# Kernel optimization log

Hardware: AMD Instinct MI355X
Metric: run time of the kernel (lower is better)

Reference implementation:

```python
import jax, jax.numpy as jnp
import numpy as np

B, L, T = 512, 512, 128
START, STOP = T - 2, T - 1   # tag_dict: '<START>'->126, '<STOP>'->127
NEG = -10000.0


def setup_inputs() -> dict:
    key = jax.random.key(0)
    k1, k2, k3, k4 = jax.random.split(key, 4)
    feats = jax.random.normal(k1, (B, L, T), dtype=jnp.float32)
    # learned transition matrix, initialized as in CRF.__init__
    trans = jax.random.normal(k2, (T, T), dtype=jnp.float32)
    trans = trans.at[START, :].set(NEG).at[:, STOP].set(NEG)
    tags = jax.random.randint(k3, (B, L), 0, T - 2)          # gold tags, no START/STOP
    lens = jax.random.randint(k4, (B,), 1, L + 1)            # actual lengths in [1, L]
    return {"feats": feats, "transitions": trans, "tags": tags, "lens": lens}


def _crf_loss(feats, transitions, tags, lens):
    Bn, Ln, Tn = feats.shape

    # ---- forward algorithm (log partition) ----
    init = jnp.full((Tn,), NEG, dtype=feats.dtype).at[START].set(0.0)
    fv0 = jnp.broadcast_to(init, (Bn, Tn))

    def step(fv, xs):
        emit, i = xs                                  # emit: [B, T]
        # tag_var[b, next, prev] = emit[b,next] + trans[next,prev] + fv[b,prev]
        tv = emit[:, :, None] + transitions[None, :, :] + fv[:, None, :]
        new = jax.scipy.special.logsumexp(tv, axis=2)  # [B, T]
        # freeze fv once past each sentence's length (== gathering at index lens)
        fv = jnp.where((i < lens)[:, None], new, fv)
        return fv, None

    fv, _ = jax.lax.scan(step, fv0, (jnp.swapaxes(feats, 0, 1), jnp.arange(Ln)))
    terminal = fv + transitions[START][None, :]       # matches original (uses START row)
    forward_score = jax.scipy.special.logsumexp(terminal, axis=1)  # [B]

    # ---- gold sentence score ----
    start_col = jnp.full((Bn, 1), START, dtype=tags.dtype)
    stop_col = jnp.full((Bn, 1), STOP, dtype=tags.dtype)
    pad_start = jnp.concatenate([start_col, tags], axis=1)   # [B, L+1]
    pad_stop = jnp.concatenate([tags, stop_col], axis=1)     # [B, L+1]
    pos = jnp.arange(Ln + 1)[None, :]
    pad_stop = jnp.where(pos >= lens[:, None], STOP, pad_stop)

    trans_terms = transitions[pad_stop, pad_start]           # [B, L+1]
    trans_sum = jnp.sum(jnp.where(pos <= lens[:, None], trans_terms, 0.0), axis=1)
    emit_terms = jnp.take_along_axis(feats, tags[:, :, None], axis=2)[..., 0]  # [B, L]
    emit_mask = jnp.arange(Ln)[None, :] < lens[:, None]
    emit_sum = jnp.sum(jnp.where(emit_mask, emit_terms, 0.0), axis=1)
    gold_score = trans_sum + emit_sum

    return jnp.mean(forward_score - gold_score)


def reference(feats, transitions, tags, lens):
    return _crf_loss(feats, transitions, tags, lens)
```

## Files before the change

### kernel.cpp

```cpp
#include <hip/hip_runtime.h>

#define Bsz 512
#define Lsz 512
#define Tsz 128
#define TAG_START 126
#define TAG_STOP 127

__device__ __forceinline__ float rl(float v, int j) {
  return __int_as_float(__builtin_amdgcn_readlane(__float_as_int(v), j));
}
__device__ __forceinline__ float wave_max(float v) {
  #pragma unroll
  for (int off = 32; off > 0; off >>= 1) v = fmaxf(v, __shfl_down(v, off, 64));
  return v;
}
__device__ __forceinline__ float wave_sum(float v) {
  #pragma unroll
  for (int off = 32; off > 0; off >>= 1) v += __shfl_down(v, off, 64);
  return v;
}

__device__ __forceinline__ void lds_barrier() {
  asm volatile("s_waitcnt lgkmcnt(0)\n\ts_barrier" ::: "memory");
}

__global__ __launch_bounds__(256, 1) void crf_fwd_kernel(
    const float* __restrict__ feats, const float* __restrict__ trans,
    const int* __restrict__ tags, const int* __restrict__ lens,
    float* __restrict__ diff_out)
{
  __shared__ float p_part[2][4][Tsz];
  __shared__ float wredA[4];
  __shared__ float wredB[4];

  const int b   = blockIdx.x;
  const int tid = threadIdx.x;
  const int w   = tid >> 6;
  const int k   = tid & 63;
  const int tagu = w * 32 + (k & 31);
  const int len = lens[b];
  const float* fb = feats + (size_t)b * Lsz * Tsz;

  float er0[32], er1[32];
  {
    const float* r0 = trans + (size_t)k * Tsz + w * 32;
    const float* r1 = trans + (size_t)(k + 64) * Tsz + w * 32;
    #pragma unroll
    for (int j = 0; j < 32; j += 4) {
      float4 a = *(const float4*)(r0 + j);
      float4 c = *(const float4*)(r1 + j);
      er0[j+0] = __expf(a.x); er0[j+1] = __expf(a.y);
      er0[j+2] = __expf(a.z); er0[j+3] = __expf(a.w);
      er1[j+0] = __expf(c.x); er1[j+1] = __expf(c.y);
      er1[j+2] = __expf(c.z); er1[j+3] = __expf(c.w);
    }
  }

  float u  = (k < 32 && tagu == TAG_START) ? 1.0f : 0.0f;
  float m  = 0.0f;
  float fv = 0.0f;

  int t1 = (1 < len) ? 1 : len - 1;
  int t2 = (2 < len) ? 2 : len - 1;
  float e0 = fb[tagu];
  float e1 = fb[(size_t)t1 * Tsz + tagu];
  float e2 = fb[(size_t)t2 * Tsz + tagu];
  int buf = 0;

  for (int t = 0; t < len; ++t) {
    int tn = t + 3; tn = (tn < len) ? tn : (len - 1);
    float e3 = fb[(size_t)tn * Tsz + tagu];
    float ee = __expf(e0);

    float a0 = 0.f, a1 = 0.f;
    #pragma unroll
    for (int j = 0; j < 32; ++j) {
      float s = rl(u, j);
      a0 = fmaf(er0[j], s, a0);
      a1 = fmaf(er1[j], s, a1);
    }
    p_part[buf][w][k]      = a0;
    p_part[buf][w][k + 64] = a1;
    lds_barrier();

    float p  = (p_part[buf][0][tagu] + p_part[buf][1][tagu])
             + (p_part[buf][2][tagu] + p_part[buf][3][tagu]);
    float p1 = (p_part[buf][0][1] + p_part[buf][1][1])
             + (p_part[buf][2][1] + p_part[buf][3][1]);

    if (t == len - 1) fv = e0 + m + __logf(p);
    u = p * __builtin_amdgcn_rcpf(p1) * ee;
    m += __logf(p1);
    e0 = e1; e1 = e2; e2 = e3;
    buf ^= 1;
  }

  float x = (k < 32) ? (fv + trans[TAG_START * Tsz + tagu]) : -1e30f;
  float wm = wave_max(x);
  if (k == 0) wredA[w] = wm;
  __syncthreads();
  float mx = fmaxf(fmaxf(wredA[0], wredA[1]), fmaxf(wredA[2], wredA[3]));
  __syncthreads();
  float se = wave_sum((k < 32) ? __expf(x - mx) : 0.0f);
  if (k == 0) wredA[w] = se;
  __syncthreads();
  float fwd_score = mx + __logf((wredA[0] + wredA[1]) + (wredA[2] + wredA[3]));

  const int* tg = tags + (size_t)b * Lsz;
  float acc = 0.0f;
  for (int pos = tid; pos <= len; pos += 256) {
    int st = (pos == 0)   ? TAG_START : tg[pos - 1];
    int et = (pos == len) ? TAG_STOP  : tg[pos];
    acc += trans[et * Tsz + st];
  }
  for (int l = tid; l < len; l += 256)
    acc += fb[(size_t)l * Tsz + tg[l]];

  float gs = wave_sum(acc);
  if (k == 0) wredB[w] = gs;
  __syncthreads();
  if (tid == 0)
    diff_out[b] = fwd_score - ((wredB[0] + wredB[1]) + (wredB[2] + wredB[3]));
}

__global__ __launch_bounds__(Bsz) void crf_final_kernel(
    const float* __restrict__ diff, float* __restrict__ out)
{
  int tid = threadIdx.x;
  float v = diff[tid];
  __shared__ float wred[8];
  float s = wave_sum(v);
  int wave = tid >> 6, lane = tid & 63;
  if (lane == 0) wred[wave] = s;
  __syncthreads();
  if (tid == 0) {
    float t = 0.f;
    #pragma unroll
    for (int i = 0; i < 8; ++i) t += wred[i];
    out[0] = t * (1.0f / Bsz);
  }
}

extern "C" void kernel_launch(void* const* d_in, const int* in_sizes, int n_in,
                              void* d_out, int out_size, void* d_ws, size_t ws_size,
                              hipStream_t stream) {
  const float* feats = (const float*)d_in[0];
  const float* trans = (const float*)d_in[1];
  const int*   tags  = (const int*)d_in[2];
  const int*   lens  = (const int*)d_in[3];
  float* out  = (float*)d_out;
  float* diff = (float*)d_ws;

  crf_fwd_kernel<<<Bsz, 256, 0, stream>>>(feats, trans, tags, lens, diff);
  crf_final_kernel<<<1, Bsz, 0, stream>>>(diff, out);
}
```

Measured before the change: 465.7 us.

## Use one wavefront per sequence with LDS-broadcast state and packed FMAs

Each batch row now runs on a single 64-lane wavefront instead of four. Every lane owns two tags and computes the full 128-term dot product against the exp-transition rows it keeps in registers. It reads the shared state vector from LDS as float4 broadcasts and uses v_pk_fma_f32 with four accumulator chains. This removes the per-step cross-wave partial-sum exchange and s_barrier. The cost is twice the FMA work per lane, and each CU holds fewer active waves to hide latency.

```diff
diff --git a/kernel.cpp b/kernel.cpp
--- a/kernel.cpp
+++ b/kernel.cpp
@@ -5,6 +5,9 @@
 #define Tsz 128
 #define TAG_START 126
 #define TAG_STOP 127
+
+typedef float v2f __attribute__((ext_vector_type(2)));
+typedef float v4f __attribute__((ext_vector_type(4)));
 
 __device__ __forceinline__ float rl(float v, int j) {
   return __int_as_float(__builtin_amdgcn_readlane(__float_as_int(v), j));
@@ -20,107 +23,106 @@
   return v;
 }
 
-__device__ __forceinline__ void lds_barrier() {
-  asm volatile("s_waitcnt lgkmcnt(0)\n\ts_barrier" ::: "memory");
+__device__ __forceinline__ v2f pk_fma(v2f a, v2f b, v2f c) {
+  v2f d;
+  asm("v_pk_fma_f32 %0, %1, %2, %3" : "=v"(d) : "v"(a), "v"(b), "v"(c));
+  return d;
 }
 
-__global__ __launch_bounds__(256, 1) void crf_fwd_kernel(
+__global__ __launch_bounds__(64, 1) void crf_fwd_kernel(
     const float* __restrict__ feats, const float* __restrict__ trans,
     const int* __restrict__ tags, const int* __restrict__ lens,
     float* __restrict__ diff_out)
 {
-  __shared__ float p_part[2][4][Tsz];
-  __shared__ float wredA[4];
-  __shared__ float wredB[4];
+  __shared__ __align__(16) float u_lds[Tsz];
 
-  const int b   = blockIdx.x;
-  const int tid = threadIdx.x;
-  const int w   = tid >> 6;
-  const int k   = tid & 63;
-  const int tagu = w * 32 + (k & 31);
+  const int b = blockIdx.x;
+  const int j = threadIdx.x;
   const int len = lens[b];
   const float* fb = feats + (size_t)b * Lsz * Tsz;
 
-  float er0[32], er1[32];
+  v2f er0[64], er1[64];
   {
-    const float* r0 = trans + (size_t)k * Tsz + w * 32;
-    const float* r1 = trans + (size_t)(k + 64) * Tsz + w * 32;
+    const v4f* r0 = (const v4f*)(trans + (size_t)j * Tsz);
+    const v4f* r1 = (const v4f*)(trans + (size_t)(j + 64) * Tsz);
     #pragma unroll
-    for (int j = 0; j < 32; j += 4) {
-      float4 a = *(const float4*)(r0 + j);
-      float4 c = *(const float4*)(r1 + j);
-      er0[j+0] = __expf(a.x); er0[j+1] = __expf(a.y);
-      er0[j+2] = __expf(a.z); er0[j+3] = __expf(a.w);
-      er1[j+0] = __expf(c.x); er1[j+1] = __expf(c.y);
-      er1[j+2] = __expf(c.z); er1[j+3] = __expf(c.w);
+    for (int i = 0; i < 32; ++i) {
+      v4f q0 = r0[i], q1 = r1[i];
+      er0[2*i]   = (v2f){__expf(q0.x), __expf(q0.y)};
+      er0[2*i+1] = (v2f){__expf(q0.z), __expf(q0.w)};
+      er1[2*i]   = (v2f){__expf(q1.x), __expf(q1.y)};
+      er1[2*i+1] = (v2f){__expf(q1.z), __expf(q1.w)};
     }
   }
 
-  float u  = (k < 32 && tagu == TAG_START) ? 1.0f : 0.0f;
-  float m  = 0.0f;
-  float fv = 0.0f;
+  u_lds[j]      = 0.0f;
+  u_lds[j + 64] = (j + 64 == TAG_START) ? 1.0f : 0.0f;
 
-  int t1 = (1 < len) ? 1 : len - 1;
-  int t2 = (2 < len) ? 2 : len - 1;
-  float e0 = fb[tagu];
-  float e1 = fb[(size_t)t1 * Tsz + tagu];
-  float e2 = fb[(size_t)t2 * Tsz + tagu];
-  int buf = 0;
+  int i1 = (1 < len) ? 1 : len - 1;
+  int i2 = (2 < len) ? 2 : len - 1;
+  int i3 = (3 < len) ? 3 : len - 1;
+  float ea0 = fb[j],                 eb0 = fb[j + 64];
+  float ea1 = fb[(size_t)i1*Tsz+j],  eb1 = fb[(size_t)i1*Tsz+j+64];
+  float ea2 = fb[(size_t)i2*Tsz+j],  eb2 = fb[(size_t)i2*Tsz+j+64];
+  float ea3 = fb[(size_t)i3*Tsz+j],  eb3 = fb[(size_t)i3*Tsz+j+64];
+
+  float m = 0.0f, fva = 0.0f, fvb = 0.0f;
 
   for (int t = 0; t < len; ++t) {
-    int tn = t + 3; tn = (tn < len) ? tn : (len - 1);
-    float e3 = fb[(size_t)tn * Tsz + tagu];
-    float ee = __expf(e0);
+    int tp = t + 4; tp = (tp < len) ? tp : (len - 1);
+    float na = fb[(size_t)tp * Tsz + j];
+    float nb = fb[(size_t)tp * Tsz + j + 64];
+    float ee0 = __expf(ea0), ee1 = __expf(eb0);
 
-    float a0 = 0.f, a1 = 0.f;
+    v2f z = (v2f){0.f, 0.f};
+    v2f a0[4] = {z, z, z, z}, a1[4] = {z, z, z, z};
+    const v4f* up = (const v4f*)u_lds;
     #pragma unroll
-    for (int j = 0; j < 32; ++j) {
-      float s = rl(u, j);
-      a0 = fmaf(er0[j], s, a0);
-      a1 = fmaf(er1[j], s, a1);
+    for (int i = 0; i < 32; ++i) {
+      v4f q = up[i];
+      v2f lo = __builtin_shufflevector(q, q, 0, 1);
+      v2f hi = __builtin_shufflevector(q, q, 2, 3);
+      a0[(2*i)   & 3] = pk_fma(er0[2*i],   lo, a0[(2*i)   & 3]);
+      a1[(2*i)   & 3] = pk_fma(er1[2*i],   lo, a1[(2*i)   & 3]);
+      a0[(2*i+1) & 3] = pk_fma(er0[2*i+1], hi, a0[(2*i+1) & 3]);
+      a1[(2*i+1) & 3] = pk_fma(er1[2*i+1], hi, a1[(2*i+1) & 3]);
     }
-    p_part[buf][w][k]      = a0;
-    p_part[buf][w][k + 64] = a1;
-    lds_barrier();
+    v2f s0 = (a0[0] + a0[1]) + (a0[2] + a0[3]);
+    v2f s1 = (a1[0] + a1[1]) + (a1[2] + a1[3]);
+    float p0 = s0.x + s0.y;
+    float p1r = s1.x + s1.y;
 
-    float p  = (p_part[buf][0][tagu] + p_part[buf][1][tagu])
-             + (p_part[buf][2][tagu] + p_part[buf][3][tagu]);
-    float p1 = (p_part[buf][0][1] + p_part[buf][1][1])
-             + (p_part[buf][2][1] + p_part[buf][3][1]);
-
-    if (t == len - 1) fv = e0 + m + __logf(p);
-    u = p * __builtin_amdgcn_rcpf(p1) * ee;
+    float p1 = rl(p0, 1);
+    float r = __builtin_amdgcn_rcpf(p1);
+    if (t == len - 1) {
+      fva = ea0 + m + __logf(p0);
+      fvb = eb0 + m + __logf(p1r);
+    }
+    u_lds[j]      = p0  * r * ee0;
+    u_lds[j + 64] = p1r * r * ee1;
     m += __logf(p1);
-    e0 = e1; e1 = e2; e2 = e3;
-    buf ^= 1;
+    ea0 = ea1; ea1 = ea2; ea2 = ea3; ea3 = na;
+    eb0 = eb1; eb1 = eb2; eb2 = eb3; eb3 = nb;
   }
 
-  float x = (k < 32) ? (fv + trans[TAG_START * Tsz + tagu]) : -1e30f;
-  float wm = wave_max(x);
-  if (k == 0) wredA[w] = wm;
-  __syncthreads();
-  float mx = fmaxf(fmaxf(wredA[0], wredA[1]), fmaxf(wredA[2], wredA[3]));
-  __syncthreads();
-  float se = wave_sum((k < 32) ? __expf(x - mx) : 0.0f);
-  if (k == 0) wredA[w] = se;
-  __syncthreads();
-  float fwd_score = mx + __logf((wredA[0] + wredA[1]) + (wredA[2] + wredA[3]));
+  float x0 = fva + trans[TAG_START * Tsz + j];
+  float x1 = fvb + trans[TAG_START * Tsz + j + 64];
+  float mx = rl(wave_max(fmaxf(x0, x1)), 0);
+  float se = rl(wave_sum(__expf(x0 - mx) + __expf(x1 - mx)), 0);
+  float fwd_score = mx + __logf(se);
 
   const int* tg = tags + (size_t)b * Lsz;
   float acc = 0.0f;
-  for (int pos = tid; pos <= len; pos += 256) {
+  for (int pos = j; pos <= len; pos += 64) {
     int st = (pos == 0)   ? TAG_START : tg[pos - 1];
     int et = (pos == len) ? TAG_STOP  : tg[pos];
     acc += trans[et * Tsz + st];
   }
-  for (int l = tid; l < len; l += 256)
+  for (int l = j; l < len; l += 64)
     acc += fb[(size_t)l * Tsz + tg[l]];
+  float gold = rl(wave_sum(acc), 0);
 
-  float gs = wave_sum(acc);
-  if (k == 0) wredB[w] = gs;
-  __syncthreads();
-  if (tid == 0)
-    diff_out[b] = fwd_score - ((wredB[0] + wredB[1]) + (wredB[2] + wredB[3]));
+  if (j == 0) diff_out[b] = fwd_score - gold;
 }
 
 __global__ __launch_bounds__(Bsz) void crf_final_kernel(
@@ -151,6 +153,6 @@
   float* out  = (float*)d_out;
   float* diff = (float*)d_ws;
 
-  crf_fwd_kernel<<<Bsz, 256, 0, stream>>>(feats, trans, tags, lens, diff);
+  crf_fwd_kernel<<<Bsz, 64, 0, stream>>>(feats, trans, tags, lens, diff);
   crf_final_kernel<<<1, Bsz, 0, stream>>>(diff, out);
 }
```

After: 955.7 us. 105% more time.

## Batch 16 sequences per block and run forward recursion on bf16 MFMA

Applied to the files above, without the earlier changes.

Each block now processes 16 sequences at once, so the per-step matrix-vector product becomes a 128x128 by 128x16 matrix multiply done with bf16 MFMA instructions, with the scaled state vectors exchanged through double-buffered LDS. Normalization now uses the first two entries of the previous state, and each sequence's final state is captured at its own length while the loop runs to the group's max length. This is meant to remove the serial FMA/readlane work and the cost of one 256-thread block per sequence. In exchange it reduces precision to bf16, launches only 32 blocks (low occupancy on the GPU), and wastes steps on sequences shorter than their group's max length.

```diff
diff --git a/kernel.cpp b/kernel.cpp
--- a/kernel.cpp
+++ b/kernel.cpp
@@ -5,122 +5,185 @@
 #define Tsz 128
 #define TAG_START 126
 #define TAG_STOP 127
-
-__device__ __forceinline__ float rl(float v, int j) {
-  return __int_as_float(__builtin_amdgcn_readlane(__float_as_int(v), j));
-}
-__device__ __forceinline__ float wave_max(float v) {
-  #pragma unroll
-  for (int off = 32; off > 0; off >>= 1) v = fmaxf(v, __shfl_down(v, off, 64));
-  return v;
-}
-__device__ __forceinline__ float wave_sum(float v) {
-  #pragma unroll
-  for (int off = 32; off > 0; off >>= 1) v += __shfl_down(v, off, 64);
-  return v;
-}
+#define SPB 16
+#define UPITCH 136
+
+typedef __attribute__((ext_vector_type(8))) short short8;
+typedef __attribute__((ext_vector_type(4))) float f32x4;
 
 __device__ __forceinline__ void lds_barrier() {
   asm volatile("s_waitcnt lgkmcnt(0)\n\ts_barrier" ::: "memory");
 }
-
-__global__ __launch_bounds__(256, 1) void crf_fwd_kernel(
+__device__ __forceinline__ unsigned pack_bf16(float lo, float hi) {
+  unsigned a = (__float_as_uint(lo) + 0x8000u) >> 16;
+  unsigned b = (__float_as_uint(hi) + 0x8000u) & 0xFFFF0000u;
+  return b | a;
+}
+__device__ __forceinline__ float bf16lo(unsigned d) { return __uint_as_float(d << 16); }
+__device__ __forceinline__ float bf16hi(unsigned d) { return __uint_as_float(d & 0xFFFF0000u); }
+
+__global__ __launch_bounds__(256) void crf_fwd_kernel(
     const float* __restrict__ feats, const float* __restrict__ trans,
     const int* __restrict__ tags, const int* __restrict__ lens,
     float* __restrict__ diff_out)
 {
-  __shared__ float p_part[2][4][Tsz];
-  __shared__ float wredA[4];
-  __shared__ float wredB[4];
-
-  const int b   = blockIdx.x;
-  const int tid = threadIdx.x;
-  const int w   = tid >> 6;
-  const int k   = tid & 63;
-  const int tagu = w * 32 + (k & 31);
-  const int len = lens[b];
-  const float* fb = feats + (size_t)b * Lsz * Tsz;
-
-  float er0[32], er1[32];
+  __shared__ __align__(16) unsigned short u_lds[2][SPB][UPITCH];
+  __shared__ float red[4][SPB];
+  __shared__ float gold_sh[SPB];
+  __shared__ int msh;
+
+  const int g    = blockIdx.x;
+  const int tid  = threadIdx.x;
+  const int w    = tid >> 6;
+  const int lane = tid & 63;
+  const int q    = lane >> 4;
+  const int s    = lane & 15;
+  const int seq  = g * SPB + s;
+  const int lenc = lens[seq];
+
+  if (tid == 0) msh = 1;
+  __syncthreads();
+  if (tid < SPB) atomicMax(&msh, lens[g * SPB + tid]);
+  for (int i = tid; i < 2 * SPB * UPITCH; i += 256)
+    ((unsigned short*)u_lds)[i] = 0;
+  __syncthreads();
+  const int maxlen = msh;
+  if (tid < SPB) u_lds[0][tid][TAG_START] = 0x3F80;
+  __syncthreads();
+
+  short8 af[2][4];
+  #pragma unroll
+  for (int i = 0; i < 2; ++i) {
+    const float* tr = trans + (size_t)((2 * w + i) * 16 + s) * Tsz + q * 8;
+    #pragma unroll
+    for (int c = 0; c < 4; ++c) {
+      float4 x = *(const float4*)(tr + c * 32);
+      float4 y = *(const float4*)(tr + c * 32 + 4);
+      union { unsigned u[4]; short8 v; } cv;
+      cv.u[0] = pack_bf16(__expf(x.x), __expf(x.y));
+      cv.u[1] = pack_bf16(__expf(x.z), __expf(x.w));
+      cv.u[2] = pack_bf16(__expf(y.x), __expf(y.y));
+      cv.u[3] = pack_bf16(__expf(y.z), __expf(y.w));
+      af[i][c] = cv.v;
+    }
+  }
+
+  unsigned off0[8];
+  #pragma unroll
+  for (int i = 0; i < 2; ++i)
+    #pragma unroll
+    for (int r = 0; r < 4; ++r)
+      off0[i * 4 + r] = (unsigned)seq * (Lsz * Tsz) + (2 * w + i) * 16 + 4 * q + r;
+
+  float pfa[8], pfb[8];
+  { int t1 = (1 < maxlen) ? 1 : 0;
+    #pragma unroll
+    for (int i = 0; i < 8; ++i) pfa[i] = feats[off0[i]];
+    #pragma unroll
+    for (int i = 0; i < 8; ++i) pfb[i] = feats[off0[i] + (unsigned)t1 * Tsz]; }
+
+  float m_run = 0.0f, mcap = 0.0f;
+  float ucap[8];
+  #pragma unroll
+  for (int i = 0; i < 8; ++i) ucap[i] = 1.0f;
+
+#define STEP(T, PF, BR, BW)                                                    \
+  { const int t_ = (T);                                                        \
+    short8 bq0 = *(const short8*)&u_lds[BR][s][0 * 32 + q * 8];                \
+    short8 bq1 = *(const short8*)&u_lds[BR][s][1 * 32 + q * 8];                \
+    short8 bq2 = *(const short8*)&u_lds[BR][s][2 * 32 + q * 8];                \
+    short8 bq3 = *(const short8*)&u_lds[BR][s][3 * 32 + q * 8];                \
+    unsigned ud = *(const unsigned*)&u_lds[BR][s][0];                          \
+    float eta = bf16lo(ud) + bf16hi(ud);                                       \
+    if (t_ == 0) eta = 1.0f;                                                   \
+    float ee[8];                                                               \
+    _Pragma("unroll") for (int i = 0; i < 8; ++i) ee[i] = __expf(PF[i]);       \
+    f32x4 acc0 = {0.f, 0.f, 0.f, 0.f}, acc1 = {0.f, 0.f, 0.f, 0.f};            \
+    acc0 = __builtin_amdgcn_mfma_f32_16x16x32_bf16(af[0][0], bq0, acc0, 0,0,0);\
+    acc1 = __builtin_amdgcn_mfma_f32_16x16x32_bf16(af[1][0], bq0, acc1, 0,0,0);\
+    acc0 = __builtin_amdgcn_mfma_f32_16x16x32_bf16(af[0][1], bq1, acc0, 0,0,0);\
+    acc1 = __builtin_amdgcn_mfma_f32_16x16x32_bf16(af[1][1], bq1, acc1, 0,0,0);\
+    acc0 = __builtin_amdgcn_mfma_f32_16x16x32_bf16(af[0][2], bq2, acc0, 0,0,0);\
+    acc1 = __builtin_amdgcn_mfma_f32_16x16x32_bf16(af[1][2], bq2, acc1, 0,0,0);\
+    acc0 = __builtin_amdgcn_mfma_f32_16x16x32_bf16(af[0][3], bq3, acc0, 0,0,0);\
+    acc1 = __builtin_amdgcn_mfma_f32_16x16x32_bf16(af[1][3], bq3, acc1, 0,0,0);\
+    int tp = t_ + 2; if (tp >= maxlen) tp = maxlen - 1;                        \
+    unsigned toff = (unsigned)tp * Tsz;                                        \
+    _Pragma("unroll") for (int i = 0; i < 8; ++i) PF[i] = feats[off0[i] + toff];\
+    float rce = __builtin_amdgcn_rcpf(eta);                                    \
+    bool capt = (t_ == lenc - 1);                                              \
+    float uv[8];                                                               \
+    _Pragma("unroll") for (int i = 0; i < 4; ++i) {                            \
+      uv[i]     = acc0[i] * rce * ee[i];                                       \
+      uv[4 + i] = acc1[i] * rce * ee[4 + i];                                   \
+    }                                                                          \
+    _Pragma("unroll") for (int i = 0; i < 8; ++i)                              \
+      ucap[i] = capt ? uv[i] : ucap[i];                                        \
+    m_run += __logf(eta);                                                      \
+    mcap = capt ? m_run : mcap;                                                \
+    unsigned short* dst = &u_lds[BW][s][0];                                    \
+    *(unsigned*)&dst[(2 * w + 0) * 16 + 4 * q]     = pack_bf16(uv[0], uv[1]);  \
+    *(unsigned*)&dst[(2 * w + 0) * 16 + 4 * q + 2] = pack_bf16(uv[2], uv[3]);  \
+    *(unsigned*)&dst[(2 * w + 1) * 16 + 4 * q]     = pack_bf16(uv[4], uv[5]);  \
+    *(unsigned*)&dst[(2 * w + 1) * 16 + 4 * q + 2] = pack_bf16(uv[6], uv[7]);  \
+    lds_barrier();                                                             \
+  }
+
+  for (int t = 0; t < maxlen; t += 2) {
+    STEP(t, pfa, 0, 1)
+    if (t + 1 < maxlen) STEP(t + 1, pfb, 1, 0)
+  }
+#undef STEP
+
+  __syncthreads();
+
+  float fvv[8];
+  #pragma unroll
+  for (int i = 0; i < 2; ++i)
+    #pragma unroll
+    for (int r = 0; r < 4; ++r) {
+      int row = (2 * w + i) * 16 + 4 * q + r;
+      fvv[i * 4 + r] = __logf(ucap[i * 4 + r]) + mcap + trans[TAG_START * Tsz + row];
+    }
+  float mx = fvv[0];
+  #pragma unroll
+  for (int i = 1; i < 8; ++i) mx = fmaxf(mx, fvv[i]);
+  mx = fmaxf(mx, __shfl_xor(mx, 16, 64));
+  mx = fmaxf(mx, __shfl_xor(mx, 32, 64));
+  if (q == 0) red[w][s] = mx;
+  __syncthreads();
+  float gmx = fmaxf(fmaxf(red[0][s], red[1][s]), fmaxf(red[2][s], red[3][s]));
+  __syncthreads();
+  float se = 0.f;
+  #pragma unroll
+  for (int i = 0; i < 8; ++i) se += __expf(fvv[i] - gmx);
+  se += __shfl_xor(se, 16, 64);
+  se += __shfl_xor(se, 32, 64);
+  if (q == 0) red[w][s] = se;
+  __syncthreads();
+  float fwd_score = gmx + __logf((red[0][s] + red[1][s]) + (red[2][s] + red[3][s]));
+
   {
-    const float* r0 = trans + (size_t)k * Tsz + w * 32;
-    const float* r1 = trans + (size_t)(k + 64) * Tsz + w * 32;
-    #pragma unroll
-    for (int j = 0; j < 32; j += 4) {
-      float4 a = *(const float4*)(r0 + j);
-      float4 c = *(const float4*)(r1 + j);
-      er0[j+0] = __expf(a.x); er0[j+1] = __expf(a.y);
-      er0[j+2] = __expf(a.z); er0[j+3] = __expf(a.w);
-      er1[j+0] = __expf(c.x); er1[j+1] = __expf(c.y);
-      er1[j+2] = __expf(c.z); er1[j+3] = __expf(c.w);
+    int jj = 4 * w + q;
+    int gs2 = g * SPB + jj;
+    int lenj = lens[gs2];
+    const int* tg = tags + (size_t)gs2 * Lsz;
+    const float* fbj = feats + (size_t)gs2 * (Lsz * Tsz);
+    float acc = 0.f;
+    for (int pos = s; pos <= lenj; pos += 16) {
+      int st = (pos == 0)    ? TAG_START : tg[pos - 1];
+      int et = (pos == lenj) ? TAG_STOP  : tg[pos];
+      acc += trans[et * Tsz + st];
     }
-  }
-
-  float u  = (k < 32 && tagu == TAG_START) ? 1.0f : 0.0f;
-  float m  = 0.0f;
-  float fv = 0.0f;
-
-  int t1 = (1 < len) ? 1 : len - 1;
-  int t2 = (2 < len) ? 2 : len - 1;
-  float e0 = fb[tagu];
-  float e1 = fb[(size_t)t1 * Tsz + tagu];
-  float e2 = fb[(size_t)t2 * Tsz + tagu];
-  int buf = 0;
-
-  for (int t = 0; t < len; ++t) {
-    int tn = t + 3; tn = (tn < len) ? tn : (len - 1);
-    float e3 = fb[(size_t)tn * Tsz + tagu];
-    float ee = __expf(e0);
-
-    float a0 = 0.f, a1 = 0.f;
-    #pragma unroll
-    for (int j = 0; j < 32; ++j) {
-      float s = rl(u, j);
-      a0 = fmaf(er0[j], s, a0);
-      a1 = fmaf(er1[j], s, a1);
-    }
-    p_part[buf][w][k]      = a0;
-    p_part[buf][w][k + 64] = a1;
-    lds_barrier();
-
-    float p  = (p_part[buf][0][tagu] + p_part[buf][1][tagu])
-             + (p_part[buf][2][tagu] + p_part[buf][3][tagu]);
-    float p1 = (p_part[buf][0][1] + p_part[buf][1][1])
-             + (p_part[buf][2][1] + p_part[buf][3][1]);
-
-    if (t == len - 1) fv = e0 + m + __logf(p);
-    u = p * __builtin_amdgcn_rcpf(p1) * ee;
-    m += __logf(p1);
-    e0 = e1; e1 = e2; e2 = e3;
-    buf ^= 1;
-  }
-
-  float x = (k < 32) ? (fv + trans[TAG_START * Tsz + tagu]) : -1e30f;
-  float wm = wave_max(x);
-  if (k == 0) wredA[w] = wm;
-  __syncthreads();
-  float mx = fmaxf(fmaxf(wredA[0], wredA[1]), fmaxf(wredA[2], wredA[3]));
-  __syncthreads();
-  float se = wave_sum((k < 32) ? __expf(x - mx) : 0.0f);
-  if (k == 0) wredA[w] = se;
-  __syncthreads();
-  float fwd_score = mx + __logf((wredA[0] + wredA[1]) + (wredA[2] + wredA[3]));
-
-  const int* tg = tags + (size_t)b * Lsz;
-  float acc = 0.0f;
-  for (int pos = tid; pos <= len; pos += 256) {
-    int st = (pos == 0)   ? TAG_START : tg[pos - 1];
-    int et = (pos == len) ? TAG_STOP  : tg[pos];
-    acc += trans[et * Tsz + st];
-  }
-  for (int l = tid; l < len; l += 256)
-    acc += fb[(size_t)l * Tsz + tg[l]];
-
-  float gs = wave_sum(acc);
-  if (k == 0) wredB[w] = gs;
-  __syncthreads();
-  if (tid == 0)
-    diff_out[b] = fwd_score - ((wredB[0] + wredB[1]) + (wredB[2] + wredB[3]));
+    for (int l = s; l < lenj; l += 16)
+      acc += fbj[(size_t)l * Tsz + tg[l]];
+    #pragma unroll
+    for (int off = 1; off < 16; off <<= 1) acc += __shfl_xor(acc, off, 64);
+    if (s == 0) gold_sh[jj] = acc;
+  }
+  __syncthreads();
+  if (w == 0 && q == 0)
+    diff_out[g * SPB + s] = fwd_score - gold_sh[s];
 }
 
 __global__ __launch_bounds__(Bsz) void crf_final_kernel(
@@ -129,9 +192,11 @@
   int tid = threadIdx.x;
   float v = diff[tid];
   __shared__ float wred[8];
-  float s = wave_sum(v);
+  float sum = v;
+  #pragma unroll
+  for (int off = 32; off > 0; off >>= 1) sum += __shfl_down(sum, off, 64);
   int wave = tid >> 6, lane = tid & 63;
-  if (lane == 0) wred[wave] = s;
+  if (lane == 0) wred[wave] = sum;
   __syncthreads();
   if (tid == 0) {
     float t = 0.f;
@@ -151,6 +216,6 @@
   float* out  = (float*)d_out;
   float* diff = (float*)d_ws;
 
-  crf_fwd_kernel<<<Bsz, 256, 0, stream>>>(feats, trans, tags, lens, diff);
+  crf_fwd_kernel<<<Bsz / SPB, 256, 0, stream>>>(feats, trans, tags, lens, diff);
   crf_final_kernel<<<1, Bsz, 0, stream>>>(diff, out);
 }
```

New measurement: 449.4 us. -3.5%, faster.
